# Kernel optimization log

Hardware: AMD Instinct MI355X
Metric: run time of the kernel (lower is better)

Reference implementation:

```python
import jax, jax.numpy as jnp
import numpy as np

N_NODES = 20000
N_EDGES = 320000

def setup_inputs() -> dict:
    key = jax.random.key(0)
    ks = jax.random.split(key, 12)
    def glorot(k, fan_in, fan_out):
        s = jnp.sqrt(6.0 / (fan_in + fan_out))
        return jax.random.uniform(k, (fan_in, fan_out), jnp.float32, -s, s)
    x = jax.random.normal(ks[0], (N_NODES, 16), jnp.float32)
    edge_index = jax.random.randint(ks[1], (2, N_EDGES), 0, N_NODES, jnp.int64)
    dims = [16, 64, 128, 256, 512, 1]
    out = {"x": x, "edge_index": edge_index}
    for i in range(5):
        out[f"W{i+1}"] = glorot(ks[2 + i], dims[i], dims[i + 1])
        out[f"b{i+1}"] = jnp.zeros((dims[i + 1],), jnp.float32)
    return out

def _prep(edge_index, n):
    # add self-loops (gcn_norm default add_self_loops=True)
    loop = jnp.arange(n, dtype=edge_index.dtype)
    row = jnp.concatenate([edge_index[0], loop])  # src
    col = jnp.concatenate([edge_index[1], loop])  # dst
    deg = jax.ops.segment_sum(jnp.ones_like(col, jnp.float32), col, num_segments=n)
    dinv = jnp.where(deg > 0, jax.lax.rsqrt(jnp.maximum(deg, 1.0)), 0.0)
    norm = dinv[row] * dinv[col]          # symmetric GCN normalization
    cnt = jnp.maximum(deg, 1.0)           # in-degree incl. self-loop, for mean aggr
    return row, col, norm, cnt

def _gcn(x, W, b, row, col, norm, cnt, n, mean_aggr):
    h = x @ W                              # [N, d_out]
    msg = norm[:, None] * h[row]           # gather + scale, [E+N, d_out]
    agg = jax.ops.segment_sum(msg, col, num_segments=n)
    if mean_aggr:
        agg = agg / cnt[:, None]
    return agg + b

def reference(x, edge_index, W1, b1, W2, b2, W3, b3, W4, b4, W5, b5):
    n = x.shape[0]
    row, col, norm, cnt = _prep(edge_index, n)
    h = jax.nn.relu(_gcn(x, W1, b1, row, col, norm, cnt, n, True))
    h = jax.nn.relu(_gcn(h, W2, b2, row, col, norm, cnt, n, True))
    h = jax.nn.relu(_gcn(h, W3, b3, row, col, norm, cnt, n, True))
    h = jax.nn.relu(_gcn(h, W4, b4, row, col, norm, cnt, n, True))
    h = _gcn(h, W5, b5, row, col, norm, cnt, n, False)  # output layer: default 'add' aggr
    return jax.nn.sigmoid(h)
```

## Files before the change

### kernel.cpp

```cpp
#include <hip/hip_runtime.h>
#include <hip/hip_bf16.h>
#include <math.h>


#define N_NODES 20000
#define N_EDGES 320000
#define ELLW 64

typedef __attribute__((ext_vector_type(8))) short short8;
typedef __attribute__((ext_vector_type(4))) float f32x4;

__device__ inline ushort f2bf(float f) {
    __hip_bfloat16 h = __float2bfloat16(f);
    return *(ushort*)&h;
}

__device__ inline float bf2f(short s) {
    union { unsigned int u; float f; } c;
    c.u = ((unsigned int)(unsigned short)s) << 16;
    return c.f;
}


__global__ void k_prep0(int* __restrict__ cnt, int n,
                        const float* __restrict__ W1, const float* __restrict__ W2,
                        const float* __restrict__ W3,
                        ushort* __restrict__ T1, ushort* __restrict__ T2,
                        ushort* __restrict__ T3) {
    int i = blockIdx.x * blockDim.x + threadIdx.x;
    if (i < n) cnt[i] = 0;
    const float* W; ushort* T; int K, N, j;
    if (i < 8192)        { W = W1; T = T1; K = 64;  N = 128; j = i; }
    else if (i < 40960)  { W = W2; T = T2; K = 128; N = 256; j = i - 8192; }
    else if (i < 172032) { W = W3; T = T3; K = 256; N = 512; j = i - 40960; }
    else return;
    int nn = j / K, kk = j - nn * K;
    T[(size_t)nn * K + kk] = f2bf(W[(size_t)kk * N + nn]);
}


__global__ void k_fill_ell(const int* __restrict__ row, const int* __restrict__ col,
                           int* __restrict__ cnt, int* __restrict__ ell, int E) {
    int e = blockIdx.x * blockDim.x + threadIdx.x;
    if (e >= E) return;
    int s = row[e], d = col[e];
    int pos = atomicAdd(&cnt[d], 1);
    ell[((size_t)d << 6) + pos] = s;
}

__global__ void k_deg(const int* __restrict__ cnt, float* __restrict__ dinv, int n) {
    int v = blockIdx.x * blockDim.x + threadIdx.x;
    if (v < n) dinv[v] = rsqrtf((float)(cnt[v] + 1));
}


__global__ __launch_bounds__(256) void k_l1_fused(const float4* __restrict__ x,
                                                  ushort* __restrict__ h_out,
                                                  const int* __restrict__ ell,
                                                  const int* __restrict__ cnt,
                                                  const float* __restrict__ dinv,
                                                  const float* __restrict__ W,
                                                  const float* __restrict__ b, int n) {
    __shared__ float sW[16 * 64];
    __shared__ float sb[64];
    __shared__ float sagg[64][17];
    int tid = threadIdx.x;
    #pragma unroll
    for (int i = tid; i < 1024; i += 256) sW[i] = W[i];
    if (tid < 64) sb[tid] = b[tid];

    int grp = tid >> 2;
    int lane = tid & 3;
    int v = blockIdx.x * 64 + grp;
    if (v < n) {
        float dv = dinv[v];
        int end = cnt[v];
        float inv_cnt = 1.0f / (float)(end + 1);
        const int* r = ell + ((size_t)v << 6);
        float4 hv = x[(size_t)v * 4 + lane];
        float4 acc = make_float4(dv * hv.x, dv * hv.y, dv * hv.z, dv * hv.w);
        int e = 0;
        for (; e + 8 <= end; e += 8) {
            int s0 = r[e],     s1 = r[e + 1], s2 = r[e + 2], s3 = r[e + 3];
            int s4 = r[e + 4], s5 = r[e + 5], s6 = r[e + 6], s7 = r[e + 7];
            float4 h0 = x[(size_t)s0 * 4 + lane];
            float4 h1 = x[(size_t)s1 * 4 + lane];
            float4 h2 = x[(size_t)s2 * 4 + lane];
            float4 h3 = x[(size_t)s3 * 4 + lane];
            float4 h4 = x[(size_t)s4 * 4 + lane];
            float4 h5 = x[(size_t)s5 * 4 + lane];
            float4 h6 = x[(size_t)s6 * 4 + lane];
            float4 h7 = x[(size_t)s7 * 4 + lane];
            float w0 = dinv[s0], w1 = dinv[s1], w2 = dinv[s2], w3 = dinv[s3];
            float w4 = dinv[s4], w5 = dinv[s5], w6 = dinv[s6], w7 = dinv[s7];
            acc.x += w0 * h0.x + w1 * h1.x + w2 * h2.x + w3 * h3.x
                   + w4 * h4.x + w5 * h5.x + w6 * h6.x + w7 * h7.x;
            acc.y += w0 * h0.y + w1 * h1.y + w2 * h2.y + w3 * h3.y
                   + w4 * h4.y + w5 * h5.y + w6 * h6.y + w7 * h7.y;
            acc.z += w0 * h0.z + w1 * h1.z + w2 * h2.z + w3 * h3.z
                   + w4 * h4.z + w5 * h5.z + w6 * h6.z + w7 * h7.z;
            acc.w += w0 * h0.w + w1 * h1.w + w2 * h2.w + w3 * h3.w
                   + w4 * h4.w + w5 * h5.w + w6 * h6.w + w7 * h7.w;
        }
        for (; e + 4 <= end; e += 4) {
            int s0 = r[e], s1 = r[e + 1], s2 = r[e + 2], s3 = r[e + 3];
            float4 h0 = x[(size_t)s0 * 4 + lane];
            float4 h1 = x[(size_t)s1 * 4 + lane];
            float4 h2 = x[(size_t)s2 * 4 + lane];
            float4 h3 = x[(size_t)s3 * 4 + lane];
            float w0 = dinv[s0], w1 = dinv[s1], w2 = dinv[s2], w3 = dinv[s3];
            acc.x += w0 * h0.x + w1 * h1.x + w2 * h2.x + w3 * h3.x;
            acc.y += w0 * h0.y + w1 * h1.y + w2 * h2.y + w3 * h3.y;
            acc.z += w0 * h0.z + w1 * h1.z + w2 * h2.z + w3 * h3.z;
            acc.w += w0 * h0.w + w1 * h1.w + w2 * h2.w + w3 * h3.w;
        }
        for (; e < end; e++) {
            int s = r[e];
            float w = dinv[s];
            float4 hs = x[(size_t)s * 4 + lane];
            acc.x += w * hs.x; acc.y += w * hs.y; acc.z += w * hs.z; acc.w += w * hs.w;
        }
        float sc = dv * inv_cnt;
        sagg[grp][lane * 4 + 0] = acc.x * sc;
        sagg[grp][lane * 4 + 1] = acc.y * sc;
        sagg[grp][lane * 4 + 2] = acc.z * sc;
        sagg[grp][lane * 4 + 3] = acc.w * sc;
    }
    __syncthreads();

    int vg = tid >> 2;
    int c0 = (tid & 3) * 16;
    int vout = blockIdx.x * 64 + vg;
    if (vout >= n) return;
    float o[16];
    #pragma unroll
    for (int jj = 0; jj < 16; jj++) o[jj] = sb[c0 + jj];
    #pragma unroll
    for (int k = 0; k < 16; k++) {
        float a = sagg[vg][k];
        #pragma unroll
        for (int jj = 0; jj < 16; jj++) o[jj] += a * sW[k * 64 + c0 + jj];
    }
    short8 p0, p1;
    #pragma unroll
    for (int jj = 0; jj < 8; jj++) p0[jj] = (short)f2bf(fmaxf(o[jj], 0.0f));
    #pragma unroll
    for (int jj = 0; jj < 8; jj++) p1[jj] = (short)f2bf(fmaxf(o[jj + 8], 0.0f));
    *(short8*)(h_out + (size_t)vout * 64 + c0) = p0;
    *(short8*)(h_out + (size_t)vout * 64 + c0 + 8) = p1;
}


__global__ void k_agg_ell_bf16(const short8* __restrict__ h, short8* __restrict__ out,
                               const int* __restrict__ ell, const int* __restrict__ cnt,
                               const float* __restrict__ dinv, int n, int g_shift) {
    int g = 1 << g_shift;
    int grp = threadIdx.x >> g_shift;
    int lane = threadIdx.x & (g - 1);
    int gpb = blockDim.x >> g_shift;
    int v = blockIdx.x * gpb + grp;
    if (v >= n) return;
    float dv = dinv[v];
    int end = cnt[v];
    float inv_cnt = 1.0f / (float)(end + 1);
    const int* r = ell + ((size_t)v << 6);

    float acc[8];
    short8 hv = h[(size_t)v * g + lane];
    #pragma unroll
    for (int i = 0; i < 8; i++) acc[i] = dv * bf2f(hv[i]);

    int e = 0;
    for (; e + 8 <= end; e += 8) {
        int s0 = r[e],     s1 = r[e + 1], s2 = r[e + 2], s3 = r[e + 3];
        int s4 = r[e + 4], s5 = r[e + 5], s6 = r[e + 6], s7 = r[e + 7];
        short8 h0 = h[(size_t)s0 * g + lane];
        short8 h1 = h[(size_t)s1 * g + lane];
        short8 h2 = h[(size_t)s2 * g + lane];
        short8 h3 = h[(size_t)s3 * g + lane];
        short8 h4 = h[(size_t)s4 * g + lane];
        short8 h5 = h[(size_t)s5 * g + lane];
        short8 h6 = h[(size_t)s6 * g + lane];
        short8 h7 = h[(size_t)s7 * g + lane];
        float w0 = dinv[s0], w1 = dinv[s1], w2 = dinv[s2], w3 = dinv[s3];
        float w4 = dinv[s4], w5 = dinv[s5], w6 = dinv[s6], w7 = dinv[s7];
        #pragma unroll
        for (int i = 0; i < 8; i++)
            acc[i] += w0 * bf2f(h0[i]) + w1 * bf2f(h1[i])
                    + w2 * bf2f(h2[i]) + w3 * bf2f(h3[i])
                    + w4 * bf2f(h4[i]) + w5 * bf2f(h5[i])
                    + w6 * bf2f(h6[i]) + w7 * bf2f(h7[i]);
    }
    for (; e + 4 <= end; e += 4) {
        int s0 = r[e], s1 = r[e + 1], s2 = r[e + 2], s3 = r[e + 3];
        short8 h0 = h[(size_t)s0 * g + lane];
        short8 h1 = h[(size_t)s1 * g + lane];
        short8 h2 = h[(size_t)s2 * g + lane];
        short8 h3 = h[(size_t)s3 * g + lane];
        float w0 = dinv[s0], w1 = dinv[s1], w2 = dinv[s2], w3 = dinv[s3];
        #pragma unroll
        for (int i = 0; i < 8; i++)
            acc[i] += w0 * bf2f(h0[i]) + w1 * bf2f(h1[i])
                    + w2 * bf2f(h2[i]) + w3 * bf2f(h3[i]);
    }
    for (; e < end; e++) {
        int s0 = r[e];
        float w0 = dinv[s0];
        short8 h0 = h[(size_t)s0 * g + lane];
        #pragma unroll
        for (int i = 0; i < 8; i++) acc[i] += w0 * bf2f(h0[i]);
    }
    float sc = dv * inv_cnt;
    short8 o;
    #pragma unroll
    for (int i = 0; i < 8; i++) o[i] = (short)f2bf(acc[i] * sc);
    out[(size_t)v * g + lane] = o;
}


__global__ __launch_bounds__(256) void k_agg_ell_sliced(
        const short8* __restrict__ h, short8* __restrict__ out,
        const int* __restrict__ ell, const int* __restrict__ cnt,
        const float* __restrict__ dinv, int n, int gfull_shift,
        int ns_shift, int tiles_per_sub) {
    int bid = blockIdx.x;
    int xcd = bid & 7;
    int t   = bid >> 3;
    if (t >= tiles_per_sub) return;
    int slice = xcd >> (3 - ns_shift);
    int sub   = xcd & ((8 >> ns_shift) - 1);

    int grp  = threadIdx.x >> 3;
    int lane = threadIdx.x & 7;
    int v = (sub * tiles_per_sub + t) * 32 + grp;
    if (v >= n) return;

    int gfull = 1 << gfull_shift;
    int fb = slice * 8 + lane;

    float dv = dinv[v];
    int end = cnt[v];
    float inv_cnt = 1.0f / (float)(end + 1);
    const int* r = ell + ((size_t)v << 6);

    float acc[8];
    short8 hv = h[((size_t)v << gfull_shift) + fb];
    #pragma unroll
    for (int i = 0; i < 8; i++) acc[i] = dv * bf2f(hv[i]);

    int e = 0;
    for (; e + 8 <= end; e += 8) {
        int s0 = r[e],     s1 = r[e + 1], s2 = r[e + 2], s3 = r[e + 3];
        int s4 = r[e + 4], s5 = r[e + 5], s6 = r[e + 6], s7 = r[e + 7];
        short8 h0 = h[((size_t)s0 << gfull_shift) + fb];
        short8 h1 = h[((size_t)s1 << gfull_shift) + fb];
        short8 h2 = h[((size_t)s2 << gfull_shift) + fb];
        short8 h3 = h[((size_t)s3 << gfull_shift) + fb];
        short8 h4 = h[((size_t)s4 << gfull_shift) + fb];
        short8 h5 = h[((size_t)s5 << gfull_shift) + fb];
        short8 h6 = h[((size_t)s6 << gfull_shift) + fb];
        short8 h7 = h[((size_t)s7 << gfull_shift) + fb];
        float w0 = dinv[s0], w1 = dinv[s1], w2 = dinv[s2], w3 = dinv[s3];
        float w4 = dinv[s4], w5 = dinv[s5], w6 = dinv[s6], w7 = dinv[s7];
        #pragma unroll
        for (int i = 0; i < 8; i++)
            acc[i] += w0 * bf2f(h0[i]) + w1 * bf2f(h1[i])
                    + w2 * bf2f(h2[i]) + w3 * bf2f(h3[i])
                    + w4 * bf2f(h4[i]) + w5 * bf2f(h5[i])
                    + w6 * bf2f(h6[i]) + w7 * bf2f(h7[i]);
    }
    for (; e + 4 <= end; e += 4) {
        int s0 = r[e], s1 = r[e + 1], s2 = r[e + 2], s3 = r[e + 3];
        short8 h0 = h[((size_t)s0 << gfull_shift) + fb];
        short8 h1 = h[((size_t)s1 << gfull_shift) + fb];
        short8 h2 = h[((size_t)s2 << gfull_shift) + fb];
        short8 h3 = h[((size_t)s3 << gfull_shift) + fb];
        float w0 = dinv[s0], w1 = dinv[s1], w2 = dinv[s2], w3 = dinv[s3];
        #pragma unroll
        for (int i = 0; i < 8; i++)
            acc[i] += w0 * bf2f(h0[i]) + w1 * bf2f(h1[i])
                    + w2 * bf2f(h2[i]) + w3 * bf2f(h3[i]);
    }
    for (; e < end; e++) {
        int s0 = r[e];
        float w0 = dinv[s0];
        short8 h0 = h[((size_t)s0 << gfull_shift) + fb];
        #pragma unroll
        for (int i = 0; i < 8; i++) acc[i] += w0 * bf2f(h0[i]);
    }
    float sc = dv * inv_cnt;
    short8 o;
    #pragma unroll
    for (int i = 0; i < 8; i++) o[i] = (short)f2bf(acc[i] * sc);
    out[((size_t)v << gfull_shift) + fb] = o;
}


#define GBM 128
#define GBN 128
#define GBK 32
#define LDSS 40

__global__ __launch_bounds__(256) void gemm_mfma(const ushort* __restrict__ A,
                                                 const ushort* __restrict__ Wt,
                                                 const float* __restrict__ bias,
                                                 ushort* __restrict__ C,
                                                 int K, int N, int do_relu) {
    __shared__ ushort As[GBM * LDSS];
    __shared__ ushort Bs[GBN * LDSS];
    int tid = threadIdx.x;
    int wave = tid >> 6;
    int lane = tid & 63;
    int wr = wave >> 1, wc = wave & 1;
    int q = lane >> 4;
    int mr = lane & 15;
    int row0 = blockIdx.y * GBM;
    int col0 = blockIdx.x * GBN;

    int sr = tid >> 2;
    int skoff = (tid & 3) * 8;

    f32x4 acc[4][4];
    #pragma unroll
    for (int i = 0; i < 4; i++)
        #pragma unroll
        for (int j = 0; j < 4; j++) acc[i][j] = (f32x4){0.f, 0.f, 0.f, 0.f};

    const short8 zero8 = {0, 0, 0, 0, 0, 0, 0, 0};
    short8 va0, va1, vb0, vb1;
    int gn0 = col0 + sr, gn1 = col0 + sr + 64;

    {
        int gk = skoff;
        bool kin = gk < K;
        va0 = kin ? *(const short8*)(A + (size_t)(row0 + sr) * K + gk) : zero8;
        va1 = kin ? *(const short8*)(A + (size_t)(row0 + sr + 64) * K + gk) : zero8;
        vb0 = (kin && gn0 < N) ? *(const short8*)(Wt + (size_t)gn0 * K + gk) : zero8;
        vb1 = (kin && gn1 < N) ? *(const short8*)(Wt + (size_t)gn1 * K + gk) : zero8;
        *(short8*)(As + sr * LDSS + skoff) = va0;
        *(short8*)(As + (sr + 64) * LDSS + skoff) = va1;
        *(short8*)(Bs + sr * LDSS + skoff) = vb0;
        *(short8*)(Bs + (sr + 64) * LDSS + skoff) = vb1;
    }
    __syncthreads();

    for (int k0 = 0;;) {
        int k1 = k0 + GBK;
        bool more = (k1 < K);
        if (more) {
            int gk = k1 + skoff;
            bool kin = gk < K;
            va0 = kin ? *(const short8*)(A + (size_t)(row0 + sr) * K + gk) : zero8;
            va1 = kin ? *(const short8*)(A + (size_t)(row0 + sr + 64) * K + gk) : zero8;
            vb0 = (kin && gn0 < N) ? *(const short8*)(Wt + (size_t)gn0 * K + gk) : zero8;
            vb1 = (kin && gn1 < N) ? *(const short8*)(Wt + (size_t)gn1 * K + gk) : zero8;
        }
        short8 afr[4], bfr[4];
        #pragma unroll
        for (int i = 0; i < 4; i++)
            afr[i] = *(const short8*)(As + (wr * 64 + i * 16 + mr) * LDSS + q * 8);
        #pragma unroll
        for (int j = 0; j < 4; j++)
            bfr[j] = *(const short8*)(Bs + (wc * 64 + j * 16 + mr) * LDSS + q * 8);
        #pragma unroll
        for (int i = 0; i < 4; i++)
            #pragma unroll
            for (int j = 0; j < 4; j++)
                acc[i][j] = __builtin_amdgcn_mfma_f32_16x16x32_bf16(afr[i], bfr[j],
                                                                    acc[i][j], 0, 0, 0);
        if (!more) break;
        __syncthreads();
        *(short8*)(As + sr * LDSS + skoff) = va0;
        *(short8*)(As + (sr + 64) * LDSS + skoff) = va1;
        *(short8*)(Bs + sr * LDSS + skoff) = vb0;
        *(short8*)(Bs + (sr + 64) * LDSS + skoff) = vb1;
        __syncthreads();
        k0 = k1;
    }

    #pragma unroll
    for (int j = 0; j < 4; j++) {
        int col = col0 + wc * 64 + j * 16 + mr;
        if (col >= N) continue;
        float bj = bias[col];
        #pragma unroll
        for (int i = 0; i < 4; i++) {
            int rbase = row0 + wr * 64 + i * 16 + q * 4;
            #pragma unroll
            for (int r = 0; r < 4; r++) {
                int grow = rbase + r;
                float v = acc[i][j][r] + bj;
                if (do_relu) v = fmaxf(v, 0.0f);
                C[(size_t)grow * N + col] = f2bf(v);
            }
        }
    }
}


__global__ void k_dot512_bf16(const short8* __restrict__ A, const float4* __restrict__ w,
                              float* __restrict__ out, int n) {
    int wv = (blockIdx.x * blockDim.x + threadIdx.x) >> 6;
    int lane = threadIdx.x & 63;
    if (wv >= n) return;
    short8 a = A[(size_t)wv * 64 + lane];
    float4 w0 = w[lane * 2], w1 = w[lane * 2 + 1];
    float acc = bf2f(a[0]) * w0.x + bf2f(a[1]) * w0.y + bf2f(a[2]) * w0.z + bf2f(a[3]) * w0.w
              + bf2f(a[4]) * w1.x + bf2f(a[5]) * w1.y + bf2f(a[6]) * w1.z + bf2f(a[7]) * w1.w;
    #pragma unroll
    for (int off = 32; off > 0; off >>= 1) acc += __shfl_down(acc, off, 64);
    if (lane == 0) out[wv] = acc;
}

__global__ void k_agg_final(const float* __restrict__ h, float* __restrict__ out,
                            const int* __restrict__ ell, const int* __restrict__ cnt,
                            const float* __restrict__ dinv, const float* __restrict__ b5,
                            int n) {
    int v = blockIdx.x * blockDim.x + threadIdx.x;
    if (v >= n) return;
    float dv = dinv[v];
    float acc = dv * h[v];
    int end = cnt[v];
    const int* r = ell + ((size_t)v << 6);
    for (int e = 0; e < end; e++) {
        int s = r[e];
        acc += dinv[s] * h[s];
    }
    float rr = dv * acc + b5[0];
    out[v] = 1.0f / (1.0f + expf(-rr));
}


extern "C" void kernel_launch(void* const* d_in, const int* in_sizes, int n_in,
                              void* d_out, int out_size, void* d_ws, size_t ws_size,
                              hipStream_t stream) {
    const float* x   = (const float*)d_in[0];
    const int*   ei  = (const int*)d_in[1];
    const float* W[5] = {(const float*)d_in[2], (const float*)d_in[4], (const float*)d_in[6],
                         (const float*)d_in[8], (const float*)d_in[10]};
    const float* b[5] = {(const float*)d_in[3], (const float*)d_in[5], (const float*)d_in[7],
                         (const float*)d_in[9], (const float*)d_in[11]};
    const int n = in_sizes[0] / 16;
    const int E = in_sizes[1] / 2;
    const int dims[6] = {16, 64, 128, 256, 512, 1};

    const int* e_row = ei;
    const int* e_col = ei + E;

    float* bufA_f = (float*)d_ws;
    float* bufB_f = bufA_f + (size_t)n * 512;
    ushort* bufA  = (ushort*)bufA_f;
    ushort* bufB  = (ushort*)bufB_f;
    int*   cnt    = (int*)(bufB_f + (size_t)n * 512);
    float* dinv   = (float*)(cnt + n);
    int*   ell    = (int*)(dinv + n);
    ushort* wt1   = (ushort*)(ell + (size_t)n * ELLW);
    ushort* wt2   = wt1 + 64 * 128;
    ushort* wt3   = wt2 + 128 * 256;
    ushort* wts[4] = {nullptr, wt1, wt2, wt3};

    const int Mpad = (n + GBM - 1) / GBM * GBM;
    const int ntiles32 = (n + 31) / 32;

    k_prep0<<<(172032 + 255) / 256, 256, 0, stream>>>(cnt, n, W[1], W[2], W[3],
                                                      wt1, wt2, wt3);
    k_fill_ell<<<(E + 255) / 256, 256, 0, stream>>>(e_row, e_col, cnt, ell, E);
    k_deg<<<(n + 255) / 256, 256, 0, stream>>>(cnt, dinv, n);

    k_l1_fused<<<(n + 63) / 64, 256, 0, stream>>>(
        (const float4*)x, bufA, ell, cnt, dinv, W[0], b[0], n);

    {
        int K = 64, Nd = 128;
        k_agg_ell_bf16<<<(n + 31) / 32, 256, 0, stream>>>(
            (const short8*)bufA, (short8*)bufB, ell, cnt, dinv, n, 3);
        dim3 ggrid((Nd + GBN - 1) / GBN, Mpad / GBM);
        gemm_mfma<<<ggrid, 256, 0, stream>>>(bufB, wts[1], b[1], bufA, K, Nd, 1);
    }

    {
        int K = 128, Nd = 256;
        int ns_shift = 1, xps = 8 >> ns_shift;
        int tps = (ntiles32 + xps - 1) / xps;
        k_agg_ell_sliced<<<8 * tps, 256, 0, stream>>>(
            (const short8*)bufA, (short8*)bufB, ell, cnt, dinv, n, 4, ns_shift, tps);
        dim3 ggrid((Nd + GBN - 1) / GBN, Mpad / GBM);
        gemm_mfma<<<ggrid, 256, 0, stream>>>(bufB, wts[2], b[2], bufA, K, Nd, 1);
    }

    {
        int K = 256, Nd = 512;
        int ns_shift = 2, xps = 8 >> ns_shift;
        int tps = (ntiles32 + xps - 1) / xps;
        k_agg_ell_sliced<<<8 * tps, 256, 0, stream>>>(
            (const short8*)bufA, (short8*)bufB, ell, cnt, dinv, n, 5, ns_shift, tps);
        dim3 ggrid((Nd + GBN - 1) / GBN, Mpad / GBM);
        gemm_mfma<<<ggrid, 256, 0, stream>>>(bufB, wts[3], b[3], bufA, K, Nd, 1);
    }

    k_dot512_bf16<<<(n * 64 + 255) / 256, 256, 0, stream>>>(
        (const short8*)bufA, (const float4*)W[4], bufB_f, n);
    k_agg_final<<<(n + 255) / 256, 256, 0, stream>>>(bufB_f, (float*)d_out, ell, cnt,
                                                     dinv, b[4], n);
}
```

Baseline: 213.8 us.

## Fuse final 512-wide dot into last GEMM epilogue, merge weight prep into ELL fill

The last-layer GEMM no longer writes its 20000x512 bf16 output. Its epilogue applies bias and ReLU, dots each row with W5, reduces across lanes with shuffles and atomically adds partial sums into a zeroed vector z. This removes a large store and the separate k_dot512 kernel that re-read it. Weight transposition is folded into k_fill_ell and z is zeroed in k_deg, which adds atomics and makes the summation order nondeterministic.

```diff
diff --git a/kernel.cpp b/kernel.cpp
--- a/kernel.cpp
+++ b/kernel.cpp
@@ -22,35 +22,38 @@
 }
 
 
-__global__ void k_prep0(int* __restrict__ cnt, int n,
-                        const float* __restrict__ W1, const float* __restrict__ W2,
-                        const float* __restrict__ W3,
-                        ushort* __restrict__ T1, ushort* __restrict__ T2,
-                        ushort* __restrict__ T3) {
+__global__ void k_zero(int* __restrict__ cnt, int n) {
     int i = blockIdx.x * blockDim.x + threadIdx.x;
     if (i < n) cnt[i] = 0;
-    const float* W; ushort* T; int K, N, j;
-    if (i < 8192)        { W = W1; T = T1; K = 64;  N = 128; j = i; }
-    else if (i < 40960)  { W = W2; T = T2; K = 128; N = 256; j = i - 8192; }
-    else if (i < 172032) { W = W3; T = T3; K = 256; N = 512; j = i - 40960; }
-    else return;
-    int nn = j / K, kk = j - nn * K;
-    T[(size_t)nn * K + kk] = f2bf(W[(size_t)kk * N + nn]);
 }
 
 
 __global__ void k_fill_ell(const int* __restrict__ row, const int* __restrict__ col,
-                           int* __restrict__ cnt, int* __restrict__ ell, int E) {
+                           int* __restrict__ cnt, int* __restrict__ ell, int E,
+                           const float* __restrict__ W2, const float* __restrict__ W3,
+                           const float* __restrict__ W4,
+                           ushort* __restrict__ T2, ushort* __restrict__ T3,
+                           ushort* __restrict__ T4) {
     int e = blockIdx.x * blockDim.x + threadIdx.x;
+    if (e < 172032) {
+        const float* W; ushort* T; int K, N, j;
+        if (e < 8192)        { W = W2; T = T2; K = 64;  N = 128; j = e; }
+        else if (e < 40960)  { W = W3; T = T3; K = 128; N = 256; j = e - 8192; }
+        else                 { W = W4; T = T4; K = 256; N = 512; j = e - 40960; }
+        int nn = j / K, kk = j - nn * K;
+        T[(size_t)nn * K + kk] = f2bf(W[(size_t)kk * N + nn]);
+    }
     if (e >= E) return;
     int s = row[e], d = col[e];
     int pos = atomicAdd(&cnt[d], 1);
     ell[((size_t)d << 6) + pos] = s;
 }
 
-__global__ void k_deg(const int* __restrict__ cnt, float* __restrict__ dinv, int n) {
+__global__ void k_deg(const int* __restrict__ cnt, float* __restrict__ dinv,
+                      float* __restrict__ z, int n, int mpad) {
     int v = blockIdx.x * blockDim.x + threadIdx.x;
     if (v < n) dinv[v] = rsqrtf((float)(cnt[v] + 1));
+    if (v < mpad) z[v] = 0.0f;
 }
 
 
@@ -235,7 +238,6 @@
     int v = (sub * tiles_per_sub + t) * 32 + grp;
     if (v >= n) return;
 
-    int gfull = 1 << gfull_shift;
     int fb = slice * 8 + lane;
 
     float dv = dinv[v];
@@ -305,6 +307,8 @@
                                                  const ushort* __restrict__ Wt,
                                                  const float* __restrict__ bias,
                                                  ushort* __restrict__ C,
+                                                 const float* __restrict__ dotw,
+                                                 float* __restrict__ z,
                                                  int K, int N, int do_relu) {
     __shared__ ushort As[GBM * LDSS];
     __shared__ ushort Bs[GBN * LDSS];
@@ -378,6 +382,32 @@
         k0 = k1;
     }
 
+    if (dotw) {
+        float bj[4], wj[4];
+        #pragma unroll
+        for (int j = 0; j < 4; j++) {
+            int col = col0 + wc * 64 + j * 16 + mr;
+            bj[j] = bias[col];
+            wj[j] = dotw[col];
+        }
+        #pragma unroll
+        for (int i = 0; i < 4; i++) {
+            #pragma unroll
+            for (int r = 0; r < 4; r++) {
+                float p = 0.0f;
+                #pragma unroll
+                for (int j = 0; j < 4; j++)
+                    p += fmaxf(acc[i][j][r] + bj[j], 0.0f) * wj[j];
+                #pragma unroll
+                for (int off = 1; off < 16; off <<= 1)
+                    p += __shfl_xor(p, off, 64);
+                if (mr == 0)
+                    atomicAdd(&z[row0 + wr * 64 + i * 16 + q * 4 + r], p);
+            }
+        }
+        return;
+    }
+
     #pragma unroll
     for (int j = 0; j < 4; j++) {
         int col = col0 + wc * 64 + j * 16 + mr;
@@ -388,29 +418,14 @@
             int rbase = row0 + wr * 64 + i * 16 + q * 4;
             #pragma unroll
             for (int r = 0; r < 4; r++) {
-                int grow = rbase + r;
                 float v = acc[i][j][r] + bj;
                 if (do_relu) v = fmaxf(v, 0.0f);
-                C[(size_t)grow * N + col] = f2bf(v);
+                C[(size_t)(rbase + r) * N + col] = f2bf(v);
             }
         }
     }
 }
 
-
-__global__ void k_dot512_bf16(const short8* __restrict__ A, const float4* __restrict__ w,
-                              float* __restrict__ out, int n) {
-    int wv = (blockIdx.x * blockDim.x + threadIdx.x) >> 6;
-    int lane = threadIdx.x & 63;
-    if (wv >= n) return;
-    short8 a = A[(size_t)wv * 64 + lane];
-    float4 w0 = w[lane * 2], w1 = w[lane * 2 + 1];
-    float acc = bf2f(a[0]) * w0.x + bf2f(a[1]) * w0.y + bf2f(a[2]) * w0.z + bf2f(a[3]) * w0.w
-              + bf2f(a[4]) * w1.x + bf2f(a[5]) * w1.y + bf2f(a[6]) * w1.z + bf2f(a[7]) * w1.w;
-    #pragma unroll
-    for (int off = 32; off > 0; off >>= 1) acc += __shfl_down(acc, off, 64);
-    if (lane == 0) out[wv] = acc;
-}
 
 __global__ void k_agg_final(const float* __restrict__ h, float* __restrict__ out,
                             const int* __restrict__ ell, const int* __restrict__ cnt,
@@ -454,18 +469,19 @@
     int*   cnt    = (int*)(bufB_f + (size_t)n * 512);
     float* dinv   = (float*)(cnt + n);
     int*   ell    = (int*)(dinv + n);
-    ushort* wt1   = (ushort*)(ell + (size_t)n * ELLW);
-    ushort* wt2   = wt1 + 64 * 128;
-    ushort* wt3   = wt2 + 128 * 256;
-    ushort* wts[4] = {nullptr, wt1, wt2, wt3};
+    ushort* wt2   = (ushort*)(ell + (size_t)n * ELLW);
+    ushort* wt3   = wt2 + 64 * 128;
+    ushort* wt4   = wt3 + 128 * 256;
+    float* z      = (float*)(wt4 + 256 * 512);
+    ushort* wts[4] = {nullptr, wt2, wt3, wt4};
 
     const int Mpad = (n + GBM - 1) / GBM * GBM;
     const int ntiles32 = (n + 31) / 32;
 
-    k_prep0<<<(172032 + 255) / 256, 256, 0, stream>>>(cnt, n, W[1], W[2], W[3],
-                                                      wt1, wt2, wt3);
-    k_fill_ell<<<(E + 255) / 256, 256, 0, stream>>>(e_row, e_col, cnt, ell, E);
-    k_deg<<<(n + 255) / 256, 256, 0, stream>>>(cnt, dinv, n);
+    k_zero<<<(n + 255) / 256, 256, 0, stream>>>(cnt, n);
+    k_fill_ell<<<(E + 255) / 256, 256, 0, stream>>>(e_row, e_col, cnt, ell, E,
+                                                    W[1], W[2], W[3], wt2, wt3, wt4);
+    k_deg<<<(Mpad + 255) / 256, 256, 0, stream>>>(cnt, dinv, z, n, Mpad);
 
     k_l1_fused<<<(n + 63) / 64, 256, 0, stream>>>(
         (const float4*)x, bufA, ell, cnt, dinv, W[0], b[0], n);
@@ -474,8 +490,9 @@
         int K = 64, Nd = 128;
         k_agg_ell_bf16<<<(n + 31) / 32, 256, 0, stream>>>(
             (const short8*)bufA, (short8*)bufB, ell, cnt, dinv, n, 3);
-        dim3 ggrid((Nd + GBN - 1) / GBN, Mpad / GBM);
-        gemm_mfma<<<ggrid, 256, 0, stream>>>(bufB, wts[1], b[1], bufA, K, Nd, 1);
+        dim3 ggrid(Nd / GBN, Mpad / GBM);
+        gemm_mfma<<<ggrid, 256, 0, stream>>>(bufB, wts[1], b[1], bufA,
+                                             nullptr, nullptr, K, Nd, 1);
     }
 
     {
@@ -484,8 +501,9 @@
         int tps = (ntiles32 + xps - 1) / xps;
         k_agg_ell_sliced<<<8 * tps, 256, 0, stream>>>(
             (const short8*)bufA, (short8*)bufB, ell, cnt, dinv, n, 4, ns_shift, tps);
-        dim3 ggrid((Nd + GBN - 1) / GBN, Mpad / GBM);
-        gemm_mfma<<<ggrid, 256, 0, stream>>>(bufB, wts[2], b[2], bufA, K, Nd, 1);
+        dim3 ggrid(Nd / GBN, Mpad / GBM);
+        gemm_mfma<<<ggrid, 256, 0, stream>>>(bufB, wts[2], b[2], bufA,
+                                             nullptr, nullptr, K, Nd, 1);
     }
 
     {
@@ -494,12 +512,11 @@
         int tps = (ntiles32 + xps - 1) / xps;
         k_agg_ell_sliced<<<8 * tps, 256, 0, stream>>>(
             (const short8*)bufA, (short8*)bufB, ell, cnt, dinv, n, 5, ns_shift, tps);
-        dim3 ggrid((Nd + GBN - 1) / GBN, Mpad / GBM);
-        gemm_mfma<<<ggrid, 256, 0, stream>>>(bufB, wts[3], b[3], bufA, K, Nd, 1);
-    }
-
-    k_dot512_bf16<<<(n * 64 + 255) / 256, 256, 0, stream>>>(
-        (const short8*)bufA, (const float4*)W[4], bufB_f, n);
-    k_agg_final<<<(n + 255) / 256, 256, 0, stream>>>(bufB_f, (float*)d_out, ell, cnt,
+        dim3 ggrid(Nd / GBN, Mpad / GBM);
+        gemm_mfma<<<ggrid, 256, 0, stream>>>(bufB, wts[3], b[3], nullptr,
+                                             W[4], z, K, Nd, 1);
+    }
+
+    k_agg_final<<<(n + 255) / 256, 256, 0, stream>>>(z, (float*)d_out, ell, cnt,
                                                      dinv, b[4], n);
 }
```

Result: faster. 208.7 us (-2.4%).
